# Optimization experiments

Hardware: AMD Instinct MI355X
Metric: run time of the kernel (lower is better)

The kernel has to match this reference:

```python
import jax, jax.numpy as jnp
import numpy as np

B, D, H, W = 32, 256, 32, 32
K = 1024

def setup_inputs() -> dict:
    key = jax.random.key(0)
    k1, k2 = jax.random.split(key)
    x = jax.random.normal(k1, (B, D, H, W), dtype=jnp.float32)
    codebook = jax.random.normal(k2, (K, D), dtype=jnp.float32)
    return {"x": x, "codebook": codebook}

def reference(x, codebook):
    b, lat, h, w = x.shape
    # (B, D, H, W) -> (B*H*W, D) tokens
    xt = jnp.transpose(x, (0, 2, 3, 1)).reshape(-1, lat)  # [N, D]
    # Squared euclidean distances via expansion (argmin-equivalent to cdist)
    x_sq = jnp.sum(xt * xt, axis=-1, keepdims=True)           # [N, 1]
    c_sq = jnp.sum(codebook * codebook, axis=-1)[None, :]     # [1, K]
    dist2 = x_sq - 2.0 * (xt @ codebook.T) + c_sq             # [N, K]
    idx = jnp.argmin(dist2, axis=-1)                          # [N]
    quant = codebook[idx]                                     # [N, D]
    codebook_loss = jnp.mean((jax.lax.stop_gradient(xt) - quant) ** 2)
    commitment_loss = jnp.mean((xt - jax.lax.stop_gradient(quant)) ** 2)
    # Straight-through estimator
    out = xt + jax.lax.stop_gradient(quant - xt)              # [N, D]
    out = out.reshape(b, h, w, lat).transpose(0, 3, 1, 2)     # [B, D, H, W]
    min_enc_idx = idx.reshape(b, h, w)                        # [B, H, W]
    return out, min_enc_idx, codebook_loss, commitment_loss
```

## Files before the change

### kernel.cpp

```cpp
#include <hip/hip_runtime.h>

#define B_   32
#define D_   256
#define HW_  1024
#define N_   32768
#define K_   1024
#define DHW  (D_ * HW_)
#define MARGIN 0.3f

typedef __attribute__((ext_vector_type(8)))  short bf16x8;
typedef __attribute__((ext_vector_type(16))) float f32x16;

union FragU { uint4 q; bf16x8 v; };

__device__ inline uint bf16rne(float x) {
    uint ub = __float_as_uint(x);
    return (ub + 0x7fffu + ((ub >> 16) & 1u)) >> 16;
}

__global__ __launch_bounds__(256)
void prep_cb(const float* __restrict__ cb, uint4* __restrict__ cbt,
             float* __restrict__ csq, float* __restrict__ cbT) {
    __shared__ uint sh[256], sl[256];
    __shared__ float rr[4];
    const int k = blockIdx.x, d = threadIdx.x;
    float v = cb[(size_t)k * D_ + d];
    uint hb = bf16rne(v);
    float hf = __uint_as_float(hb << 16);
    uint lb = bf16rne(v - hf);
    sh[d] = hb; sl[d] = lb;
    cbT[(size_t)d * K_ + k] = v;
    float s = v * v;
    #pragma unroll
    for (int off = 32; off >= 1; off >>= 1) s += __shfl_xor(s, off, 64);
    if ((d & 63) == 0) rr[d >> 6] = s;
    __syncthreads();
    if (d == 0) csq[k] = (rr[0] + rr[1]) + (rr[2] + rr[3]);
    if (d < 64) {
        int ch = d >> 3, g = d & 7;
        int p = g >> 2, gg = g & 3;
        const uint* src = p ? sl : sh;
        uint w[4];
        #pragma unroll
        for (int jj = 0; jj < 4; ++jj) {
            int dp = ch * 16 + gg * 4 + jj;
            w[jj] = src[2 * dp] | (src[2 * dp + 1] << 16);
        }
        cbt[(size_t)(ch * 1024 + k) * 8 + g] = make_uint4(w[0], w[1], w[2], w[3]);
    }
}

__global__ __launch_bounds__(512)
void vq_main(const float* __restrict__ x, const uint4* __restrict__ cbt,
             const float* __restrict__ csqg, int* __restrict__ bestk,
             int* __restrict__ rcount, int* __restrict__ rlist,
             float* __restrict__ bdist) {
    __shared__ uint4 TkS[4096];
    __shared__ uint4 CbS[2][2048];
    __shared__ float csqS[1024];

    const int tid = threadIdx.x;
    const int lane = tid & 63;
    const int sub = lane >> 5, l31 = lane & 31;
    const int wid = tid >> 6;
    const int wm = wid >> 1, wn = wid & 1;
    const int tok0 = blockIdx.x * 128;
    const int bb = tok0 >> 10, hw0 = tok0 & 1023;

    csqS[tid] = csqg[tid];
    csqS[tid + 512] = csqg[tid + 512];

    {
        const int t = tid & 127;
        const int dgrp = tid >> 7;
        const float* xp = x + (size_t)bb * DHW + hw0 + t;
        #pragma unroll
        for (int i = 0; i < 8; ++i) {
            int g = i * 4 + dgrp;
            float v[8];
            #pragma unroll
            for (int e = 0; e < 8; ++e)
                v[e] = xp[(size_t)(g * 8 + e) * HW_];
            uint w[4];
            #pragma unroll
            for (int jj = 0; jj < 4; ++jj)
                w[jj] = bf16rne(v[2 * jj]) | (bf16rne(v[2 * jj + 1]) << 16);
            TkS[t * 32 + (g ^ (t & 7))] = make_uint4(w[0], w[1], w[2], w[3]);
        }
    }
    asm volatile("s_waitcnt vmcnt(0) lgkmcnt(0)" ::: "memory");
    __syncthreads();

    const int s_cl = tid >> 3;
    const int s_g = (tid & 7) ^ (s_cl & 7);

    #pragma unroll
    for (int it = 0; it < 4; ++it) {
        int u = it * 512 + tid;
        int cl = it * 64 + s_cl;
        const uint4* src = cbt + (size_t)cl * 8 + s_g;
        __builtin_amdgcn_global_load_lds((const uint*)src, (uint*)&CbS[0][u], 16, 0, 0);
    }

    f32x16 acc[2][2] = {};
    float v1[2] = {3.4e38f, 3.4e38f}, v2[2] = {3.4e38f, 3.4e38f};
    int k1[2] = {0, 0};

    int cur = 0;
    for (int cc = 0; cc < 32; ++cc) {
        asm volatile("s_barrier" ::: "memory");
        if (cc + 1 < 32) {
            const int nct = (cc + 1) >> 3, nch = (cc + 1) & 7;
            #pragma unroll
            for (int it = 0; it < 4; ++it) {
                int u = it * 512 + tid;
                int cl = it * 64 + s_cl;
                const uint4* src = cbt + (size_t)(nch * 1024 + nct * 256 + cl) * 8 + s_g;
                __builtin_amdgcn_global_load_lds((const uint*)src, (uint*)&CbS[cur ^ 1][u], 16, 0, 0);
            }
            asm volatile("s_waitcnt vmcnt(4)" ::: "memory");
        } else {
            asm volatile("s_waitcnt vmcnt(0)" ::: "memory");
        }
        asm volatile("s_barrier" ::: "memory");

        const int ch = cc & 7;
        #pragma unroll
        for (int ks = 0; ks < 2; ++ks) {
            FragU tf[2], cfh[2], cfl[2];
            #pragma unroll
            for (int j = 0; j < 2; ++j) {
                int t = wn * 64 + j * 32 + l31;
                int g32 = ch * 4 + ks * 2 + sub;
                tf[j].q = TkS[t * 32 + (g32 ^ (t & 7))];
            }
            #pragma unroll
            for (int f = 0; f < 2; ++f) {
                int cl = wm * 64 + f * 32 + l31;
                int gh = ks * 2 + sub;
                int gl = 4 + ks * 2 + sub;
                cfh[f].q = CbS[cur][cl * 8 + (gh ^ (cl & 7))];
                cfl[f].q = CbS[cur][cl * 8 + (gl ^ (cl & 7))];
            }
            #pragma unroll
            for (int f = 0; f < 2; ++f)
                #pragma unroll
                for (int j = 0; j < 2; ++j)
                    acc[f][j] = __builtin_amdgcn_mfma_f32_32x32x16_bf16(cfh[f].v, tf[j].v, acc[f][j], 0, 0, 0);
            #pragma unroll
            for (int f = 0; f < 2; ++f)
                #pragma unroll
                for (int j = 0; j < 2; ++j)
                    acc[f][j] = __builtin_amdgcn_mfma_f32_32x32x16_bf16(cfl[f].v, tf[j].v, acc[f][j], 0, 0, 0);
        }
        cur ^= 1;

        if ((cc & 7) == 7) {
            const int ct = cc >> 3;
            const int cbase = ct * 256 + wm * 64 + sub * 4;
            #pragma unroll
            for (int f = 0; f < 2; ++f) {
                #pragma unroll
                for (int g8 = 0; g8 < 4; ++g8) {
                    float4 cs4 = *reinterpret_cast<const float4*>(&csqS[cbase + f * 32 + g8 * 8]);
                    const float csa[4] = {cs4.x, cs4.y, cs4.z, cs4.w};
                    #pragma unroll
                    for (int q = 0; q < 4; ++q) {
                        int code = cbase + f * 32 + g8 * 8 + q;
                        int r = g8 * 4 + q;
                        #pragma unroll
                        for (int j = 0; j < 2; ++j) {
                            float s = fmaf(-2.f, acc[f][j][r], csa[q]);
                            bool c = s < v1[j];
                            v2[j] = c ? v1[j] : fminf(v2[j], s);
                            k1[j] = c ? code : k1[j];
                            v1[j] = c ? s : v1[j];
                        }
                    }
                }
            }
            const f32x16 zf = {};
            #pragma unroll
            for (int f = 0; f < 2; ++f)
                #pragma unroll
                for (int j = 0; j < 2; ++j) acc[f][j] = zf;
        }
    }

    #pragma unroll
    for (int j = 0; j < 2; ++j) {
        float ov1 = __shfl_xor(v1[j], 32, 64);
        float ov2 = __shfl_xor(v2[j], 32, 64);
        int   ok1 = __shfl_xor(k1[j], 32, 64);
        float nv2 = fminf(fminf(v2[j], ov2), fmaxf(v1[j], ov1));
        if (ov1 < v1[j] || (ov1 == v1[j] && ok1 < k1[j])) { v1[j] = ov1; k1[j] = ok1; }
        v2[j] = nv2;
    }
    __syncthreads();
    float* red = (float*)&CbS[0][0];
    if (sub == 0) {
        #pragma unroll
        for (int j = 0; j < 2; ++j) {
            int t = wn * 64 + j * 32 + l31;
            red[(wm * 128 + t) * 4 + 0] = v1[j];
            red[(wm * 128 + t) * 4 + 1] = v2[j];
            red[(wm * 128 + t) * 4 + 2] = __int_as_float(k1[j]);
        }
    }
    __syncthreads();
    if (tid < 128) {
        float bv1 = red[tid * 4], bv2 = red[tid * 4 + 1];
        int bk = __float_as_int(red[tid * 4 + 2]);
        #pragma unroll
        for (int m = 1; m < 4; ++m) {
            float a1 = red[(m * 128 + tid) * 4], a2 = red[(m * 128 + tid) * 4 + 1];
            int ak = __float_as_int(red[(m * 128 + tid) * 4 + 2]);
            float nv2 = fminf(fminf(bv2, a2), fmaxf(bv1, a1));
            if (a1 < bv1 || (a1 == bv1 && ak < bk)) { bv1 = a1; bk = ak; }
            bv2 = nv2;
        }
        int n = tok0 + tid;
        bestk[n] = bk;
        bdist[n] = bv1;
        if (bv2 - bv1 < MARGIN) rlist[atomicAdd(rcount, 1)] = n;
    }
}

__global__ __launch_bounds__(256)
void vq_refine(const float* __restrict__ x, const float* __restrict__ cbT,
               const float* __restrict__ csq, const int* __restrict__ rcount,
               const int* __restrict__ rlist, int* __restrict__ bestk,
               float* __restrict__ bdist) {
    __shared__ float xv[8][256];
    __shared__ float xsq[8];
    __shared__ float wredv[4][8];
    __shared__ int   wredk[4][8];
    const int tid = threadIdx.x;
    const int cnt = min(rcount[0], N_);
    for (int base = blockIdx.x * 8; base < cnt; base += gridDim.x * 8) {
        const int m = min(8, cnt - base);
        __syncthreads();
        for (int j = 0; j < m; ++j) {
            int n = rlist[base + j];
            int b = n >> 10, hw = n & 1023;
            xv[j][tid] = x[(size_t)b * DHW + (size_t)tid * HW_ + hw];
        }
        for (int j = m; j < 8; ++j) xv[j][tid] = 0.f;
        __syncthreads();
        {
            int g = tid >> 5, l = tid & 31;
            float s = 0.f;
            #pragma unroll
            for (int d8 = 0; d8 < 8; ++d8) { float v = xv[g][d8 * 32 + l]; s = fmaf(v, v, s); }
            #pragma unroll
            for (int mm = 1; mm < 32; mm <<= 1) s += __shfl_xor(s, mm, 64);
            if (l == 0) xsq[g] = s;
        }
        __syncthreads();

        float dots[4][8];
        #pragma unroll
        for (int c4 = 0; c4 < 4; ++c4)
            #pragma unroll
            for (int j = 0; j < 8; ++j) dots[c4][j] = 0.f;

        const float* cbase = cbT + tid;
        for (int d0 = 0; d0 < 256; d0 += 8) {
            float xr[8][8];
            #pragma unroll
            for (int j = 0; j < 8; ++j) {
                float4 a = *reinterpret_cast<const float4*>(&xv[j][d0]);
                float4 b = *reinterpret_cast<const float4*>(&xv[j][d0 + 4]);
                xr[j][0] = a.x; xr[j][1] = a.y; xr[j][2] = a.z; xr[j][3] = a.w;
                xr[j][4] = b.x; xr[j][5] = b.y; xr[j][6] = b.z; xr[j][7] = b.w;
            }
            #pragma unroll
            for (int c4 = 0; c4 < 4; ++c4) {
                float cv[8];
                #pragma unroll
                for (int u = 0; u < 8; ++u)
                    cv[u] = cbase[(size_t)(d0 + u) * K_ + c4 * 256];
                #pragma unroll
                for (int u = 0; u < 8; ++u)
                    #pragma unroll
                    for (int j = 0; j < 8; ++j)
                        dots[c4][j] = fmaf(cv[u], xr[j][u], dots[c4][j]);
            }
        }

        float bv[8]; int bk[8];
        #pragma unroll
        for (int j = 0; j < 8; ++j) { bv[j] = 3.4e38f; bk[j] = 0; }
        #pragma unroll
        for (int c4 = 0; c4 < 4; ++c4) {
            const int code = c4 * 256 + tid;
            const float cs = csq[code];
            #pragma unroll
            for (int j = 0; j < 8; ++j) {
                float dist = fmaf(-2.f, dots[c4][j], xsq[j]) + cs;
                if (dist < bv[j]) { bv[j] = dist; bk[j] = code; }
            }
        }
        #pragma unroll
        for (int j = 0; j < 8; ++j) {
            if (j < m) {
                float v = bv[j]; int k = bk[j];
                #pragma unroll
                for (int mm = 1; mm < 64; mm <<= 1) {
                    float ov = __shfl_xor(v, mm, 64);
                    int   ok = __shfl_xor(k, mm, 64);
                    if (ov < v || (ov == v && ok < k)) { v = ov; k = ok; }
                }
                if ((tid & 63) == 0) { wredv[tid >> 6][j] = v; wredk[tid >> 6][j] = k; }
            }
        }
        __syncthreads();
        if (tid < m) {
            float v = wredv[0][tid]; int k = wredk[0][tid];
            #pragma unroll
            for (int q = 1; q < 4; ++q) {
                if (wredv[q][tid] < v || (wredv[q][tid] == v && wredk[q][tid] < k)) {
                    v = wredv[q][tid]; k = wredk[q][tid];
                }
            }
            int n = rlist[base + tid];
            bestk[n] = k;
            bdist[n] = v;
        }
        __syncthreads();
    }
}

__global__ __launch_bounds__(256)
void vq_gather(const float* __restrict__ cb, const int* __restrict__ bestk,
               const float* __restrict__ bdist, float* __restrict__ out,
               float* __restrict__ oidx, float* __restrict__ oloss) {
    const int n0 = blockIdx.x * 64;
    const int tid = threadIdx.x;
    const int j = tid & 63, dg = tid >> 6;
    const int n = n0 + j;
    const int b = n >> 10, hw = n & 1023;
    const int k = bestk[n];
    const float* cw = cb + (size_t)k * D_;
    const size_t basex = (size_t)b * DHW + hw;
    #pragma unroll 4
    for (int d = dg * 64; d < dg * 64 + 64; ++d) {
        out[basex + (size_t)d * HW_] = cw[d];
    }
    if (tid < 64) {
        oidx[n0 + tid] = (float)bestk[n0 + tid];
        float v = bdist[n0 + tid];
        #pragma unroll
        for (int off = 32; off >= 1; off >>= 1) v += __shfl_xor(v, off, 64);
        if (tid == 0) {
            float t = v * (1.0f / 8388608.0f);
            atomicAdd(&oloss[0], t);
            atomicAdd(&oloss[1], t);
        }
    }
}

extern "C" void kernel_launch(void* const* d_in, const int* in_sizes, int n_in,
                              void* d_out, int out_size, void* d_ws, size_t ws_size,
                              hipStream_t stream) {
    const float* x  = (const float*)d_in[0];
    const float* cb = (const float*)d_in[1];

    float* out   = (float*)d_out;
    float* oidx  = out + 8388608;
    float* oloss = out + 8388608 + 32768;

    uint* wsb = (uint*)d_ws;
    uint4*  cbt   = (uint4*)wsb;
    float*  csq   = (float*)(wsb + 262144);
    float*  cbT   = (float*)(wsb + 263168);
    int*    bestk = (int*)  (wsb + 525312);
    int*    rcount= (int*)  (wsb + 558080);
    int*    rlist = (int*)  (wsb + 558084);
    float*  bdist = (float*)(wsb + 590852);

    hipMemsetAsync(rcount, 0, sizeof(int), stream);
    hipMemsetAsync(oloss, 0, 2 * sizeof(float), stream);

    prep_cb <<<1024, 256, 0, stream>>>(cb, cbt, csq, cbT);
    vq_main <<<256, 512, 0, stream>>>(x, cbt, csq, bestk, rcount, rlist, bdist);
    vq_refine<<<256, 256, 0, stream>>>(x, cbT, csq, rcount, rlist, bestk, bdist);
    vq_gather<<<512, 256, 0, stream>>>(cb, bestk, bdist, out, oidx, oloss);
}
```

Before: 130.2 us.

## Retile VQ GEMM per-wave, drop transposed codebook copy, fold memsets into prep

Each wave in the main distance kernel now covers all 128 tokens against 64 codes, with token fragments loaded once per chunk. The codebook and token LDS layouts are changed to plain row-major planes with no XOR swizzle, and codebook chunks are 512 codes by 16 d-steps. The loop also gains setprio hints and a two-blocks-per-CU launch bound. The separate transposed fp32 codebook and the two hipMemsetAsync calls are removed: refine now reads the original codebook row-wise with float4 loads, and prep_cb zeroes the counters. The gather writes float4 outputs per four tokens. These changes risk LDS bank conflicts from the unswizzled layout and higher register pressure from eight accumulators per wave.

```diff
diff --git a/kernel.cpp b/kernel.cpp
--- a/kernel.cpp
+++ b/kernel.cpp
@@ -19,8 +19,9 @@
 }
 
 __global__ __launch_bounds__(256)
-void prep_cb(const float* __restrict__ cb, uint4* __restrict__ cbt,
-             float* __restrict__ csq, float* __restrict__ cbT) {
+void prep_cb(const float* __restrict__ cb, uint4* __restrict__ cbt2,
+             float* __restrict__ csq, int* __restrict__ rcount,
+             float* __restrict__ oloss) {
     __shared__ uint sh[256], sl[256];
     __shared__ float rr[4];
     const int k = blockIdx.x, d = threadIdx.x;
@@ -29,41 +30,39 @@
     float hf = __uint_as_float(hb << 16);
     uint lb = bf16rne(v - hf);
     sh[d] = hb; sl[d] = lb;
-    cbT[(size_t)d * K_ + k] = v;
     float s = v * v;
     #pragma unroll
     for (int off = 32; off >= 1; off >>= 1) s += __shfl_xor(s, off, 64);
     if ((d & 63) == 0) rr[d >> 6] = s;
     __syncthreads();
     if (d == 0) csq[k] = (rr[0] + rr[1]) + (rr[2] + rr[3]);
+    if (k == 0 && d == 0) { *rcount = 0; oloss[0] = 0.f; oloss[1] = 0.f; }
     if (d < 64) {
-        int ch = d >> 3, g = d & 7;
-        int p = g >> 2, gg = g & 3;
+        const int ch = d >> 2, it = d & 3;
+        const int p = it >> 1, h = it & 1;
+        const int d0 = ch * 16 + h * 8;
         const uint* src = p ? sl : sh;
         uint w[4];
         #pragma unroll
-        for (int jj = 0; jj < 4; ++jj) {
-            int dp = ch * 16 + gg * 4 + jj;
-            w[jj] = src[2 * dp] | (src[2 * dp + 1] << 16);
-        }
-        cbt[(size_t)(ch * 1024 + k) * 8 + g] = make_uint4(w[0], w[1], w[2], w[3]);
-    }
-}
-
-__global__ __launch_bounds__(512)
-void vq_main(const float* __restrict__ x, const uint4* __restrict__ cbt,
+        for (int jj = 0; jj < 4; ++jj)
+            w[jj] = src[d0 + 2 * jj] | (src[d0 + 2 * jj + 1] << 16);
+        cbt2[((ch * 4 + it) << 10) + k] = make_uint4(w[0], w[1], w[2], w[3]);
+    }
+}
+
+__global__ __launch_bounds__(512, 2)
+void vq_main(const float* __restrict__ x, const uint4* __restrict__ cbt2,
              const float* __restrict__ csqg, int* __restrict__ bestk,
              int* __restrict__ rcount, int* __restrict__ rlist,
              float* __restrict__ bdist) {
-    __shared__ uint4 TkS[4096];
-    __shared__ uint4 CbS[2][2048];
+    __shared__ uint4 TkS[32][128];
+    __shared__ uint4 CbS[2][4][512];
     __shared__ float csqS[1024];
 
     const int tid = threadIdx.x;
     const int lane = tid & 63;
     const int sub = lane >> 5, l31 = lane & 31;
-    const int wid = tid >> 6;
-    const int wm = wid >> 1, wn = wid & 1;
+    const int wm = tid >> 6;
     const int tok0 = blockIdx.x * 128;
     const int bb = tok0 >> 10, hw0 = tok0 & 1023;
 
@@ -85,38 +84,39 @@
             #pragma unroll
             for (int jj = 0; jj < 4; ++jj)
                 w[jj] = bf16rne(v[2 * jj]) | (bf16rne(v[2 * jj + 1]) << 16);
-            TkS[t * 32 + (g ^ (t & 7))] = make_uint4(w[0], w[1], w[2], w[3]);
+            TkS[g][t] = make_uint4(w[0], w[1], w[2], w[3]);
         }
     }
     asm volatile("s_waitcnt vmcnt(0) lgkmcnt(0)" ::: "memory");
     __syncthreads();
 
-    const int s_cl = tid >> 3;
-    const int s_g = (tid & 7) ^ (s_cl & 7);
-
     #pragma unroll
     for (int it = 0; it < 4; ++it) {
-        int u = it * 512 + tid;
-        int cl = it * 64 + s_cl;
-        const uint4* src = cbt + (size_t)cl * 8 + s_g;
-        __builtin_amdgcn_global_load_lds((const uint*)src, (uint*)&CbS[0][u], 16, 0, 0);
-    }
-
-    f32x16 acc[2][2] = {};
-    float v1[2] = {3.4e38f, 3.4e38f}, v2[2] = {3.4e38f, 3.4e38f};
-    int k1[2] = {0, 0};
+        const uint4* src = cbt2 + ((it << 10) + tid);
+        __builtin_amdgcn_global_load_lds((const uint*)src, (uint*)&CbS[0][it][tid], 16, 0, 0);
+    }
+
+    f32x16 acc[2][4] = {};
+    float v1[4], v2[4]; int k1[4];
+    #pragma unroll
+    for (int j = 0; j < 4; ++j) { v1[j] = 3.4e38f; v2[j] = 3.4e38f; k1[j] = 0; }
 
     int cur = 0;
     for (int cc = 0; cc < 32; ++cc) {
+        const int ct = cc >> 4, ch = cc & 15;
+
+        FragU tf[4];
+        #pragma unroll
+        for (int j = 0; j < 4; ++j)
+            tf[j].q = TkS[ch * 2 + sub][j * 32 + l31];
+
         asm volatile("s_barrier" ::: "memory");
         if (cc + 1 < 32) {
-            const int nct = (cc + 1) >> 3, nch = (cc + 1) & 7;
+            const int nct = (cc + 1) >> 4, nch = (cc + 1) & 15;
             #pragma unroll
             for (int it = 0; it < 4; ++it) {
-                int u = it * 512 + tid;
-                int cl = it * 64 + s_cl;
-                const uint4* src = cbt + (size_t)(nch * 1024 + nct * 256 + cl) * 8 + s_g;
-                __builtin_amdgcn_global_load_lds((const uint*)src, (uint*)&CbS[cur ^ 1][u], 16, 0, 0);
+                const uint4* src = cbt2 + (((nch * 4 + it) << 10) + nct * 512 + tid);
+                __builtin_amdgcn_global_load_lds((const uint*)src, (uint*)&CbS[cur ^ 1][it][tid], 16, 0, 0);
             }
             asm volatile("s_waitcnt vmcnt(4)" ::: "memory");
         } else {
@@ -124,40 +124,29 @@
         }
         asm volatile("s_barrier" ::: "memory");
 
-        const int ch = cc & 7;
-        #pragma unroll
-        for (int ks = 0; ks < 2; ++ks) {
-            FragU tf[2], cfh[2], cfl[2];
-            #pragma unroll
-            for (int j = 0; j < 2; ++j) {
-                int t = wn * 64 + j * 32 + l31;
-                int g32 = ch * 4 + ks * 2 + sub;
-                tf[j].q = TkS[t * 32 + (g32 ^ (t & 7))];
-            }
-            #pragma unroll
-            for (int f = 0; f < 2; ++f) {
-                int cl = wm * 64 + f * 32 + l31;
-                int gh = ks * 2 + sub;
-                int gl = 4 + ks * 2 + sub;
-                cfh[f].q = CbS[cur][cl * 8 + (gh ^ (cl & 7))];
-                cfl[f].q = CbS[cur][cl * 8 + (gl ^ (cl & 7))];
-            }
-            #pragma unroll
-            for (int f = 0; f < 2; ++f)
-                #pragma unroll
-                for (int j = 0; j < 2; ++j)
-                    acc[f][j] = __builtin_amdgcn_mfma_f32_32x32x16_bf16(cfh[f].v, tf[j].v, acc[f][j], 0, 0, 0);
-            #pragma unroll
-            for (int f = 0; f < 2; ++f)
-                #pragma unroll
-                for (int j = 0; j < 2; ++j)
-                    acc[f][j] = __builtin_amdgcn_mfma_f32_32x32x16_bf16(cfl[f].v, tf[j].v, acc[f][j], 0, 0, 0);
-        }
+        FragU cfh[2], cfl[2];
+        #pragma unroll
+        for (int f = 0; f < 2; ++f) {
+            int c = wm * 64 + f * 32 + l31;
+            cfh[f].q = CbS[cur][sub][c];
+            cfl[f].q = CbS[cur][2 + sub][c];
+        }
+        __builtin_amdgcn_s_setprio(1);
+        #pragma unroll
+        for (int f = 0; f < 2; ++f)
+            #pragma unroll
+            for (int j = 0; j < 4; ++j)
+                acc[f][j] = __builtin_amdgcn_mfma_f32_32x32x16_bf16(cfh[f].v, tf[j].v, acc[f][j], 0, 0, 0);
+        #pragma unroll
+        for (int f = 0; f < 2; ++f)
+            #pragma unroll
+            for (int j = 0; j < 4; ++j)
+                acc[f][j] = __builtin_amdgcn_mfma_f32_32x32x16_bf16(cfl[f].v, tf[j].v, acc[f][j], 0, 0, 0);
+        __builtin_amdgcn_s_setprio(0);
         cur ^= 1;
 
-        if ((cc & 7) == 7) {
-            const int ct = cc >> 3;
-            const int cbase = ct * 256 + wm * 64 + sub * 4;
+        if (ch == 15) {
+            const int cbase = ct * 512 + wm * 64 + sub * 4;
             #pragma unroll
             for (int f = 0; f < 2; ++f) {
                 #pragma unroll
@@ -169,7 +158,7 @@
                         int code = cbase + f * 32 + g8 * 8 + q;
                         int r = g8 * 4 + q;
                         #pragma unroll
-                        for (int j = 0; j < 2; ++j) {
+                        for (int j = 0; j < 4; ++j) {
                             float s = fmaf(-2.f, acc[f][j][r], csa[q]);
                             bool c = s < v1[j];
                             v2[j] = c ? v1[j] : fminf(v2[j], s);
@@ -183,12 +172,12 @@
             #pragma unroll
             for (int f = 0; f < 2; ++f)
                 #pragma unroll
-                for (int j = 0; j < 2; ++j) acc[f][j] = zf;
-        }
-    }
-
-    #pragma unroll
-    for (int j = 0; j < 2; ++j) {
+                for (int j = 0; j < 4; ++j) acc[f][j] = zf;
+        }
+    }
+
+    #pragma unroll
+    for (int j = 0; j < 4; ++j) {
         float ov1 = __shfl_xor(v1[j], 32, 64);
         float ov2 = __shfl_xor(v2[j], 32, 64);
         int   ok1 = __shfl_xor(k1[j], 32, 64);
@@ -197,24 +186,24 @@
         v2[j] = nv2;
     }
     __syncthreads();
-    float* red = (float*)&CbS[0][0];
+    float* red = (float*)&CbS[0][0][0];
     if (sub == 0) {
         #pragma unroll
-        for (int j = 0; j < 2; ++j) {
-            int t = wn * 64 + j * 32 + l31;
-            red[(wm * 128 + t) * 4 + 0] = v1[j];
-            red[(wm * 128 + t) * 4 + 1] = v2[j];
-            red[(wm * 128 + t) * 4 + 2] = __int_as_float(k1[j]);
+        for (int j = 0; j < 4; ++j) {
+            int t = j * 32 + l31;
+            red[(wm * 128 + t) * 3 + 0] = v1[j];
+            red[(wm * 128 + t) * 3 + 1] = v2[j];
+            red[(wm * 128 + t) * 3 + 2] = __int_as_float(k1[j]);
         }
     }
     __syncthreads();
     if (tid < 128) {
-        float bv1 = red[tid * 4], bv2 = red[tid * 4 + 1];
-        int bk = __float_as_int(red[tid * 4 + 2]);
-        #pragma unroll
-        for (int m = 1; m < 4; ++m) {
-            float a1 = red[(m * 128 + tid) * 4], a2 = red[(m * 128 + tid) * 4 + 1];
-            int ak = __float_as_int(red[(m * 128 + tid) * 4 + 2]);
+        float bv1 = red[tid * 3], bv2 = red[tid * 3 + 1];
+        int bk = __float_as_int(red[tid * 3 + 2]);
+        #pragma unroll
+        for (int m = 1; m < 8; ++m) {
+            float a1 = red[(m * 128 + tid) * 3], a2 = red[(m * 128 + tid) * 3 + 1];
+            int ak = __float_as_int(red[(m * 128 + tid) * 3 + 2]);
             float nv2 = fminf(fminf(bv2, a2), fmaxf(bv1, a1));
             if (a1 < bv1 || (a1 == bv1 && ak < bk)) { bv1 = a1; bk = ak; }
             bv2 = nv2;
@@ -227,7 +216,7 @@
 }
 
 __global__ __launch_bounds__(256)
-void vq_refine(const float* __restrict__ x, const float* __restrict__ cbT,
+void vq_refine(const float* __restrict__ x, const float* __restrict__ cb,
                const float* __restrict__ csq, const int* __restrict__ rcount,
                const int* __restrict__ rlist, int* __restrict__ bestk,
                float* __restrict__ bdist) {
@@ -264,7 +253,6 @@
             #pragma unroll
             for (int j = 0; j < 8; ++j) dots[c4][j] = 0.f;
 
-        const float* cbase = cbT + tid;
         for (int d0 = 0; d0 < 256; d0 += 8) {
             float xr[8][8];
             #pragma unroll
@@ -276,10 +264,10 @@
             }
             #pragma unroll
             for (int c4 = 0; c4 < 4; ++c4) {
-                float cv[8];
-                #pragma unroll
-                for (int u = 0; u < 8; ++u)
-                    cv[u] = cbase[(size_t)(d0 + u) * K_ + c4 * 256];
+                const float4* cr = reinterpret_cast<const float4*>(
+                    cb + (size_t)(c4 * 256 + tid) * D_ + d0);
+                float4 ca = cr[0], cbv = cr[1];
+                float cv[8] = { ca.x, ca.y, ca.z, ca.w, cbv.x, cbv.y, cbv.z, cbv.w };
                 #pragma unroll
                 for (int u = 0; u < 8; ++u)
                     #pragma unroll
@@ -337,15 +325,20 @@
                float* __restrict__ oidx, float* __restrict__ oloss) {
     const int n0 = blockIdx.x * 64;
     const int tid = threadIdx.x;
-    const int j = tid & 63, dg = tid >> 6;
-    const int n = n0 + j;
-    const int b = n >> 10, hw = n & 1023;
-    const int k = bestk[n];
-    const float* cw = cb + (size_t)k * D_;
-    const size_t basex = (size_t)b * DHW + hw;
+    const int j16 = tid & 15, dg = tid >> 4;
+    const int bb = n0 >> 10, hw0 = n0 & 1023;
+    int k4[4];
+    #pragma unroll
+    for (int e = 0; e < 4; ++e) k4[e] = bestk[n0 + j16 * 4 + e];
+    const size_t obase = (size_t)bb * DHW + hw0 + j16 * 4;
     #pragma unroll 4
-    for (int d = dg * 64; d < dg * 64 + 64; ++d) {
-        out[basex + (size_t)d * HW_] = cw[d];
+    for (int d = dg * 16; d < dg * 16 + 16; ++d) {
+        float4 w;
+        w.x = cb[(size_t)k4[0] * D_ + d];
+        w.y = cb[(size_t)k4[1] * D_ + d];
+        w.z = cb[(size_t)k4[2] * D_ + d];
+        w.w = cb[(size_t)k4[3] * D_ + d];
+        *reinterpret_cast<float4*>(out + obase + (size_t)d * HW_) = w;
     }
     if (tid < 64) {
         oidx[n0 + tid] = (float)bestk[n0 + tid];
@@ -371,19 +364,15 @@
     float* oloss = out + 8388608 + 32768;
 
     uint* wsb = (uint*)d_ws;
-    uint4*  cbt   = (uint4*)wsb;
+    uint4*  cbt2  = (uint4*)wsb;
     float*  csq   = (float*)(wsb + 262144);
-    float*  cbT   = (float*)(wsb + 263168);
-    int*    bestk = (int*)  (wsb + 525312);
-    int*    rcount= (int*)  (wsb + 558080);
-    int*    rlist = (int*)  (wsb + 558084);
-    float*  bdist = (float*)(wsb + 590852);
-
-    hipMemsetAsync(rcount, 0, sizeof(int), stream);
-    hipMemsetAsync(oloss, 0, 2 * sizeof(float), stream);
-
-    prep_cb <<<1024, 256, 0, stream>>>(cb, cbt, csq, cbT);
-    vq_main <<<256, 512, 0, stream>>>(x, cbt, csq, bestk, rcount, rlist, bdist);
-    vq_refine<<<256, 256, 0, stream>>>(x, cbT, csq, rcount, rlist, bestk, bdist);
+    int*    bestk = (int*)  (wsb + 263168);
+    int*    rcount= (int*)  (wsb + 295936);
+    int*    rlist = (int*)  (wsb + 295940);
+    float*  bdist = (float*)(wsb + 328708);
+
+    prep_cb <<<1024, 256, 0, stream>>>(cb, cbt2, csq, rcount, oloss);
+    vq_main <<<256, 512, 0, stream>>>(x, cbt2, csq, bestk, rcount, rlist, bdist);
+    vq_refine<<<256, 256, 0, stream>>>(x, cb, csq, rcount, rlist, bestk, bdist);
     vq_gather<<<512, 256, 0, stream>>>(cb, bestk, bdist, out, oidx, oloss);
 }
```

Result: slower. 135.5 us (+4.0%).
